# Kernel optimization log

Hardware: AMD Instinct MI355X
Metric: run time of the kernel (lower is better)

The kernel has to match this reference:

```python
import jax, jax.numpy as jnp
import numpy as np


def setup_inputs() -> dict:
    key = jax.random.key(0)
    x = jax.random.normal(key, (4, 4096, 64), dtype=jnp.float32)
    return {"x": x}


def reference(x) -> jnp.ndarray:
    # self-attention with q = k = v = x, shape [B, S, D]
    d = x.shape[-1]
    scale = 1.0 / jnp.sqrt(jnp.asarray(d, dtype=x.dtype))
    logits = jnp.einsum('bqd,bkd->bqk', x, x) * scale  # [B, S, S]
    attn = jax.nn.softmax(logits, axis=-1)
    return jnp.einsum('bqk,bkd->bqd', attn, x)
```

## Files before the change

kernel.cpp:

```cpp
#include <hip/hip_runtime.h>
#include <cstdint>


#define SB 4096
#define DDIM 64

typedef __attribute__((ext_vector_type(16))) float f32x16;
typedef __attribute__((ext_vector_type(8)))  float f32x8;
typedef __attribute__((ext_vector_type(4)))  float f32x4;
typedef __attribute__((ext_vector_type(8)))  short bf16x8;

static __device__ __forceinline__ unsigned short bf16_rne(float f) {
  union { float f; uint32_t u; } v; v.f = f;
  uint32_t u = v.u + 0x7FFFu + ((v.u >> 16) & 1u);
  return (unsigned short)(u >> 16);
}
static __device__ __forceinline__ float bf16_tof(unsigned short h) {
  union { uint32_t u; float f; } v; v.u = ((uint32_t)h) << 16;
  return v.f;
}
static __device__ __forceinline__ f32x16 MFMA(bf16x8 a, bf16x8 b, f32x16 c) {
  return __builtin_amdgcn_mfma_f32_32x32x16_bf16(a, b, c, 0, 0, 0);
}

#define KSTRIDE 272
#define VSTRIDE 144
#define VOFF    8704
#define WREG    17920

__global__ __launch_bounds__(512, 1)
void sdpa_kernel(const float* __restrict__ x, float* __restrict__ out) {
  __shared__ __align__(16) char smem[143360];
  const int tid  = threadIdx.x;
  const int wv   = tid >> 6;
  const int lane = tid & 63;
  const int l31  = lane & 31;
  const int h5   = lane >> 5;
  const int bid  = blockIdx.x;
  const int b    = bid >> 6;
  const int q0   = (bid & 63) << 6;
  const float* __restrict__ xb = x + (size_t)b * (SB * DDIM);
  char* __restrict__ wl = smem + (size_t)wv * WREG;

  const float NEG = -3.0e38f;

  bf16x8 qh[2][4], ql[2][4];
#pragma unroll
  for (int qf = 0; qf < 2; ++qf) {
#pragma unroll
    for (int dc = 0; dc < 4; ++dc) {
      const float* p = xb + (size_t)(q0 + qf * 32 + l31) * DDIM + dc * 16 + h5 * 8;
      f32x4 a = *(const f32x4*)p;
      f32x4 c = *(const f32x4*)(p + 4);
      float v[8] = {a[0], a[1], a[2], a[3], c[0], c[1], c[2], c[3]};
#pragma unroll
      for (int j = 0; j < 8; ++j) {
        float sv = v[j] * 0.125f;
        unsigned short hi = bf16_rne(sv);
        qh[qf][dc][j] = (short)hi;
        ql[qf][dc][j] = (short)bf16_rne(sv - bf16_tof(hi));
      }
    }
  }

  f32x16 ot[2][2] = {};
  float mrun[2] = {NEG, NEG};
  float lrun[2] = {0.f, 0.f};

  const int kv0 = wv * (SB / 8);
  const int r0  = (lane >> 3) * 4;
  const int d0g = (lane & 7) * 8;

  const int vc  = r0 >> 4;
  const int vko = r0 & 15;
  const int vsA = ((vko >> 2) & 1) * 8 + ((vko >> 3) & 1) * 4;
  const uint32_t vcolb = (uint32_t)(vc * 16 + vsA) * 2;

#pragma unroll 1
  for (int st = 0; st < 16; ++st) {
    const int krow0 = kv0 + st * 32;

    bf16x8 hv[4], lv[4];
#pragma unroll
    for (int i = 0; i < 4; ++i) {
      f32x8 t = *(const f32x8*)(xb + (size_t)(krow0 + r0 + i) * DDIM + d0g);
#pragma unroll
      for (int j = 0; j < 8; ++j) {
        unsigned short hi = bf16_rne(t[j]);
        hv[i][j] = (short)hi;
        lv[i][j] = (short)bf16_rne(t[j] - bf16_tof(hi));
      }
      const int row = r0 + i;
      *(bf16x8*)(wl + row * KSTRIDE + d0g * 2)       = hv[i];
      *(bf16x8*)(wl + row * KSTRIDE + 128 + d0g * 2) = lv[i];
    }
#pragma unroll
    for (int dd = 0; dd < 8; ++dd) {
      const int d = d0g + dd;
      const uint32_t sw = ((uint32_t)((d >> 3) & 7)) << 4;
      char* rb = wl + VOFF + (uint32_t)d * VSTRIDE;
      short4 pa = make_short4(hv[0][dd], hv[1][dd], hv[2][dd], hv[3][dd]);
      short4 pb = make_short4(lv[0][dd], lv[1][dd], lv[2][dd], lv[3][dd]);
      *(short4*)(rb + (vcolb ^ sw))          = pa;
      *(short4*)(rb + ((64 + vcolb) ^ sw))   = pb;
    }

    bf16x8 kh[4], kl[4];
    {
      char* krow = wl + l31 * KSTRIDE;
#pragma unroll
      for (int dc = 0; dc < 4; ++dc) {
        const uint32_t off = (uint32_t)(dc * 32 + h5 * 16);
        kh[dc] = *(bf16x8*)(krow + off);
        kl[dc] = *(bf16x8*)(krow + 128 + off);
      }
    }
    f32x16 s0 = {}, s1 = {};
#pragma unroll
    for (int dc = 0; dc < 4; ++dc) {
      s0 = MFMA(kh[dc], qh[0][dc], s0);
      s1 = MFMA(kh[dc], qh[1][dc], s1);
      s0 = MFMA(kh[dc], ql[0][dc], s0);
      s1 = MFMA(kh[dc], ql[1][dc], s1);
      s0 = MFMA(kl[dc], qh[0][dc], s0);
      s1 = MFMA(kl[dc], qh[1][dc], s1);
    }

    bf16x8 ph[2][2], pl[2][2];
#pragma unroll
    for (int qf = 0; qf < 2; ++qf) {
      f32x16 sv = qf ? s1 : s0;
      float pm = sv[0];
#pragma unroll
      for (int r = 1; r < 16; ++r) pm = fmaxf(pm, sv[r]);
      pm = fmaxf(pm, __shfl_xor(pm, 32));
      const float mnew = fmaxf(mrun[qf], pm);
      const float corr = __expf(mrun[qf] - mnew);
      mrun[qf] = mnew;
      lrun[qf] *= corr;
#pragma unroll
      for (int df = 0; df < 2; ++df)
#pragma unroll
        for (int r = 0; r < 16; ++r) ot[qf][df][r] *= corr;
      float p[16]; float ps = 0.f;
#pragma unroll
      for (int r = 0; r < 16; ++r) { p[r] = __expf(sv[r] - mnew); ps += p[r]; }
      lrun[qf] += ps;
#pragma unroll
      for (int c = 0; c < 2; ++c)
#pragma unroll
        for (int j = 0; j < 8; ++j) {
          float pv = p[c * 8 + j];
          unsigned short hi = bf16_rne(pv);
          ph[qf][c][j] = (short)hi;
          pl[qf][c][j] = (short)bf16_rne(pv - bf16_tof(hi));
        }
    }

#pragma unroll
    for (int df = 0; df < 2; ++df) {
      const int d = df * 32 + l31;
      char* rb = wl + VOFF + (uint32_t)d * VSTRIDE;
      const uint32_t sw = ((uint32_t)((d >> 3) & 7)) << 4;
      bf16x8 vh[2], vl2[2];
#pragma unroll
      for (int c = 0; c < 2; ++c) {
        const uint32_t off = (uint32_t)(c * 32 + h5 * 16);
        vh[c]  = *(bf16x8*)(rb + (off ^ sw));
        vl2[c] = *(bf16x8*)(rb + ((64 + off) ^ sw));
      }
#pragma unroll
      for (int qf = 0; qf < 2; ++qf)
#pragma unroll
        for (int c = 0; c < 2; ++c) {
          ot[qf][df] = MFMA(vh[c],  ph[qf][c], ot[qf][df]);
          ot[qf][df] = MFMA(vh[c],  pl[qf][c], ot[qf][df]);
          ot[qf][df] = MFMA(vl2[c], ph[qf][c], ot[qf][df]);
        }
    }
  }

#pragma unroll
  for (int qf = 0; qf < 2; ++qf) lrun[qf] += __shfl_xor(lrun[qf], 32);

  __syncthreads();
  if (wv > 0) {
    char* rbase = smem + (size_t)(wv - 1) * 17408 + (size_t)lane * 272;
#pragma unroll
    for (int qf = 0; qf < 2; ++qf)
#pragma unroll
      for (int df = 0; df < 2; ++df)
#pragma unroll
        for (int t = 0; t < 4; ++t) {
          f32x4 o = { ot[qf][df][t*4+0], ot[qf][df][t*4+1],
                      ot[qf][df][t*4+2], ot[qf][df][t*4+3] };
          *(f32x4*)(rbase + (qf * 128 + df * 64 + t * 16)) = o;
        }
    f32x4 stv = { mrun[0], lrun[0], mrun[1], lrun[1] };
    *(f32x4*)(rbase + 256) = stv;
  }
  __syncthreads();
  if (wv == 0) {
#pragma unroll 1
    for (int w = 1; w < 8; ++w) {
      char* rbase = smem + (size_t)(w - 1) * 17408 + (size_t)lane * 272;
      f32x4 stv = *(f32x4*)(rbase + 256);
#pragma unroll
      for (int qf = 0; qf < 2; ++qf) {
        const float mw = stv[qf * 2 + 0];
        const float lw = stv[qf * 2 + 1];
        const float mn = fmaxf(mrun[qf], mw);
        const float f0 = __expf(mrun[qf] - mn);
        const float f1 = __expf(mw - mn);
        mrun[qf] = mn;
        lrun[qf] = lrun[qf] * f0 + lw * f1;
#pragma unroll
        for (int df = 0; df < 2; ++df)
#pragma unroll
          for (int t = 0; t < 4; ++t) {
            f32x4 o = *(f32x4*)(rbase + (qf * 128 + df * 64 + t * 16));
#pragma unroll
            for (int e = 0; e < 4; ++e)
              ot[qf][df][t*4+e] = ot[qf][df][t*4+e] * f0 + o[e] * f1;
          }
      }
    }
#pragma unroll
    for (int qf = 0; qf < 2; ++qf) {
      const float inv = 1.0f / lrun[qf];
      const size_t rowoff = ((size_t)b * SB + q0 + qf * 32 + l31) * DDIM;
#pragma unroll
      for (int df = 0; df < 2; ++df)
#pragma unroll
        for (int t = 0; t < 4; ++t) {
          const int dbase = df * 32 + t * 8 + h5 * 4;
          f32x4 o = { ot[qf][df][t*4+0] * inv, ot[qf][df][t*4+1] * inv,
                      ot[qf][df][t*4+2] * inv, ot[qf][df][t*4+3] * inv };
          *(f32x4*)(out + rowoff + dbase) = o;
        }
    }
  }
}

extern "C" void kernel_launch(void* const* d_in, const int* in_sizes, int n_in,
                              void* d_out, int out_size, void* d_ws, size_t ws_size,
                              hipStream_t stream) {
  (void)in_sizes; (void)n_in; (void)out_size; (void)d_ws; (void)ws_size;
  const float* x = (const float*)d_in[0];
  float* o = (float*)d_out;
  sdpa_kernel<<<dim3(256), dim3(512), 0, stream>>>(x, o);
}
```

Before: 125.9 us.

## Precompute bf16 hi/lo split K and transposed V into workspace

Adds a precompute kernel that converts x once into split bf16 hi/lo K rows and transposed V arrays in a workspace buffer. The main attention kernel then loads MFMA operands straight from global memory, with no per-tile conversion, LDS staging or transposes, and remaps blocks so that each XCD works on a single batch for L2 locality. The work per block drops, but it costs an extra launch, 8MB of workspace traffic and global loads with no LDS reuse. If the workspace is too small, the old kernel runs instead.

```diff
diff --git a/kernel.cpp b/kernel.cpp
--- a/kernel.cpp
+++ b/kernel.cpp
@@ -23,13 +23,257 @@
   return __builtin_amdgcn_mfma_f32_32x32x16_bf16(a, b, c, 0, 0, 0);
 }
 
+#define KF_BYTES  (4u << 20)
+#define VT_BYTES  (2u << 20)
+#define WS_NEEDED (8u << 20)
+
+__device__ __constant__ int g_koff[16] = {0,1,2,3, 8,9,10,11, 4,5,6,7, 12,13,14,15};
+
+__global__ __launch_bounds__(256)
+void precompute_kernel(const float* __restrict__ x, char* __restrict__ ws) {
+  const int bid = blockIdx.x;
+  const int tid = threadIdx.x;
+  char* __restrict__ kfmt = ws;
+  char* __restrict__ vthi = ws + KF_BYTES;
+  char* __restrict__ vtlo = ws + KF_BYTES + VT_BYTES;
+  if (bid < 512) {
+    const int t   = bid * 256 + tid;
+    const int row = t >> 3;
+    const int seg = t & 7;
+    f32x8 v = *(const f32x8*)(x + (size_t)row * 64 + seg * 8);
+    bf16x8 h, l;
+#pragma unroll
+    for (int j = 0; j < 8; ++j) {
+      unsigned short hi = bf16_rne(v[j]);
+      h[j] = (short)hi;
+      l[j] = (short)bf16_rne(v[j] - bf16_tof(hi));
+    }
+    char* dst = kfmt + (size_t)row * 256 + seg * 16;
+    *(bf16x8*)dst         = h;
+    *(bf16x8*)(dst + 128) = l;
+  } else {
+    const int w = (bid - 512) * 4 + (tid >> 6);
+    const int b = w >> 8;
+    const int c = w & 255;
+    const int d = tid & 63;
+    unsigned short hs[16], ls[16];
+#pragma unroll
+    for (int s = 0; s < 16; ++s) {
+      const int k = c * 16 + g_koff[s];
+      float v = x[((size_t)(b * SB + k)) * 64 + d];
+      hs[s] = bf16_rne(v);
+      ls[s] = bf16_rne(v - bf16_tof(hs[s]));
+    }
+    bf16x8 h0, h1, l0, l1;
+#pragma unroll
+    for (int j = 0; j < 8; ++j) {
+      h0[j] = (short)hs[j];     h1[j] = (short)hs[j + 8];
+      l0[j] = (short)ls[j];     l1[j] = (short)ls[j + 8];
+    }
+    char* dh = vthi + (size_t)(b * 64 + d) * 8192 + c * 32;
+    char* dl = vtlo + (size_t)(b * 64 + d) * 8192 + c * 32;
+    *(bf16x8*)dh = h0; *(bf16x8*)(dh + 16) = h1;
+    *(bf16x8*)dl = l0; *(bf16x8*)(dl + 16) = l1;
+  }
+}
+
+__global__ __launch_bounds__(512, 2)
+void sdpa_main(const float* __restrict__ x, const char* __restrict__ ws,
+               float* __restrict__ out) {
+  __shared__ __align__(16) char smem[121856];
+  const int tid  = threadIdx.x;
+  const int wv   = tid >> 6;
+  const int lane = tid & 63;
+  const int l31  = lane & 31;
+  const int h5   = lane >> 5;
+
+  const int p    = blockIdx.x;
+  const int xcd  = p & 7;
+  const int slot = p >> 3;
+  const int b    = xcd >> 1;
+  const int q0   = ((xcd & 1) * 32 + slot) * 64;
+
+  const float* __restrict__ xb = x + (size_t)b * (SB * DDIM);
+  const char* __restrict__ kfmt = ws;
+  const char* __restrict__ vthi = ws + KF_BYTES;
+  const char* __restrict__ vtlo = ws + KF_BYTES + VT_BYTES;
+
+  const float NEG = -3.0e38f;
+
+  bf16x8 qh[2][4], ql[2][4];
+#pragma unroll
+  for (int qf = 0; qf < 2; ++qf) {
+#pragma unroll
+    for (int dc = 0; dc < 4; ++dc) {
+      const float* ptr = xb + (size_t)(q0 + qf * 32 + l31) * DDIM + dc * 16 + h5 * 8;
+      f32x4 a = *(const f32x4*)ptr;
+      f32x4 c = *(const f32x4*)(ptr + 4);
+      float v[8] = {a[0], a[1], a[2], a[3], c[0], c[1], c[2], c[3]};
+#pragma unroll
+      for (int j = 0; j < 8; ++j) {
+        float sv = v[j] * 0.125f;
+        unsigned short hi = bf16_rne(sv);
+        qh[qf][dc][j] = (short)hi;
+        ql[qf][dc][j] = (short)bf16_rne(sv - bf16_tof(hi));
+      }
+    }
+  }
+
+  f32x16 ot[2][2] = {};
+  float mrun[2] = {NEG, NEG};
+  float lrun[2] = {0.f, 0.f};
+
+  const int kv0 = wv * (SB / 8);
+
+  const char* kbase = kfmt + (size_t)(b * SB + kv0 + l31) * 256 + h5 * 16;
+  const char* vbh   = vthi + (size_t)(b * 64 + l31) * 8192 + (size_t)kv0 * 2 + h5 * 16;
+  const char* vbl   = vtlo + (size_t)(b * 64 + l31) * 8192 + (size_t)kv0 * 2 + h5 * 16;
+
+#pragma unroll 1
+  for (int st = 0; st < 16; ++st) {
+    bf16x8 kh[4], kl[4];
+#pragma unroll
+    for (int dc = 0; dc < 4; ++dc) {
+      kh[dc] = *(const bf16x8*)(kbase + dc * 32);
+      kl[dc] = *(const bf16x8*)(kbase + 128 + dc * 32);
+    }
+
+    f32x16 s0 = {}, s1 = {};
+#pragma unroll
+    for (int dc = 0; dc < 4; ++dc) {
+      s0 = MFMA(kh[dc], qh[0][dc], s0);
+      s1 = MFMA(kh[dc], qh[1][dc], s1);
+      s0 = MFMA(kh[dc], ql[0][dc], s0);
+      s1 = MFMA(kh[dc], ql[1][dc], s1);
+      s0 = MFMA(kl[dc], qh[0][dc], s0);
+      s1 = MFMA(kl[dc], qh[1][dc], s1);
+    }
+
+    bf16x8 vh[2][2], vl[2][2];
+#pragma unroll
+    for (int df = 0; df < 2; ++df)
+#pragma unroll
+      for (int c = 0; c < 2; ++c) {
+        vh[df][c] = *(const bf16x8*)(vbh + (size_t)df * (32 * 8192) + c * 32);
+        vl[df][c] = *(const bf16x8*)(vbl + (size_t)df * (32 * 8192) + c * 32);
+      }
+
+    bf16x8 ph[2][2], pl[2][2];
+#pragma unroll
+    for (int qf = 0; qf < 2; ++qf) {
+      f32x16 sv = qf ? s1 : s0;
+      float pm = sv[0];
+#pragma unroll
+      for (int r = 1; r < 16; ++r) pm = fmaxf(pm, sv[r]);
+      pm = fmaxf(pm, __shfl_xor(pm, 32));
+      const float mnew = fmaxf(mrun[qf], pm);
+      const float corr = __expf(mrun[qf] - mnew);
+      mrun[qf] = mnew;
+      lrun[qf] *= corr;
+#pragma unroll
+      for (int df = 0; df < 2; ++df)
+#pragma unroll
+        for (int r = 0; r < 16; ++r) ot[qf][df][r] *= corr;
+      float pv[16]; float ps = 0.f;
+#pragma unroll
+      for (int r = 0; r < 16; ++r) { pv[r] = __expf(sv[r] - mnew); ps += pv[r]; }
+      lrun[qf] += ps;
+#pragma unroll
+      for (int c = 0; c < 2; ++c)
+#pragma unroll
+        for (int j = 0; j < 8; ++j) {
+          float pvv = pv[c * 8 + j];
+          unsigned short hi = bf16_rne(pvv);
+          ph[qf][c][j] = (short)hi;
+          pl[qf][c][j] = (short)bf16_rne(pvv - bf16_tof(hi));
+        }
+    }
+
+#pragma unroll
+    for (int df = 0; df < 2; ++df)
+#pragma unroll
+      for (int qf = 0; qf < 2; ++qf)
+#pragma unroll
+        for (int c = 0; c < 2; ++c) {
+          ot[qf][df] = MFMA(vh[df][c], ph[qf][c], ot[qf][df]);
+          ot[qf][df] = MFMA(vh[df][c], pl[qf][c], ot[qf][df]);
+          ot[qf][df] = MFMA(vl[df][c], ph[qf][c], ot[qf][df]);
+        }
+
+    kbase += 32 * 256;
+    vbh   += 64;
+    vbl   += 64;
+  }
+
+#pragma unroll
+  for (int qf = 0; qf < 2; ++qf) lrun[qf] += __shfl_xor(lrun[qf], 32);
+
+  __syncthreads();
+  if (wv > 0) {
+    char* rbase = smem + (size_t)(wv - 1) * 17408 + (size_t)lane * 272;
+#pragma unroll
+    for (int qf = 0; qf < 2; ++qf)
+#pragma unroll
+      for (int df = 0; df < 2; ++df)
+#pragma unroll
+        for (int t = 0; t < 4; ++t) {
+          f32x4 o = { ot[qf][df][t*4+0], ot[qf][df][t*4+1],
+                      ot[qf][df][t*4+2], ot[qf][df][t*4+3] };
+          *(f32x4*)(rbase + (qf * 128 + df * 64 + t * 16)) = o;
+        }
+    f32x4 stv = { mrun[0], lrun[0], mrun[1], lrun[1] };
+    *(f32x4*)(rbase + 256) = stv;
+  }
+  __syncthreads();
+  if (wv == 0) {
+#pragma unroll 1
+    for (int w = 1; w < 8; ++w) {
+      char* rbase = smem + (size_t)(w - 1) * 17408 + (size_t)lane * 272;
+      f32x4 stv = *(f32x4*)(rbase + 256);
+#pragma unroll
+      for (int qf = 0; qf < 2; ++qf) {
+        const float mw = stv[qf * 2 + 0];
+        const float lw = stv[qf * 2 + 1];
+        const float mn = fmaxf(mrun[qf], mw);
+        const float f0 = __expf(mrun[qf] - mn);
+        const float f1 = __expf(mw - mn);
+        mrun[qf] = mn;
+        lrun[qf] = lrun[qf] * f0 + lw * f1;
+#pragma unroll
+        for (int df = 0; df < 2; ++df)
+#pragma unroll
+          for (int t = 0; t < 4; ++t) {
+            f32x4 o = *(f32x4*)(rbase + (qf * 128 + df * 64 + t * 16));
+#pragma unroll
+            for (int e = 0; e < 4; ++e)
+              ot[qf][df][t*4+e] = ot[qf][df][t*4+e] * f0 + o[e] * f1;
+          }
+      }
+    }
+#pragma unroll
+    for (int qf = 0; qf < 2; ++qf) {
+      const float inv = 1.0f / lrun[qf];
+      const size_t rowoff = ((size_t)b * SB + q0 + qf * 32 + l31) * DDIM;
+#pragma unroll
+      for (int df = 0; df < 2; ++df)
+#pragma unroll
+        for (int t = 0; t < 4; ++t) {
+          const int dbase = df * 32 + t * 8 + h5 * 4;
+          f32x4 o = { ot[qf][df][t*4+0] * inv, ot[qf][df][t*4+1] * inv,
+                      ot[qf][df][t*4+2] * inv, ot[qf][df][t*4+3] * inv };
+          *(f32x4*)(out + rowoff + dbase) = o;
+        }
+    }
+  }
+}
+
 #define KSTRIDE 272
 #define VSTRIDE 144
 #define VOFF    8704
 #define WREG    17920
 
 __global__ __launch_bounds__(512, 1)
-void sdpa_kernel(const float* __restrict__ x, float* __restrict__ out) {
+void sdpa_fb(const float* __restrict__ x, float* __restrict__ out) {
   __shared__ __align__(16) char smem[143360];
   const int tid  = threadIdx.x;
   const int wv   = tid >> 6;
@@ -41,17 +285,16 @@
   const int q0   = (bid & 63) << 6;
   const float* __restrict__ xb = x + (size_t)b * (SB * DDIM);
   char* __restrict__ wl = smem + (size_t)wv * WREG;
-
   const float NEG = -3.0e38f;
 
   bf16x8 qh[2][4], ql[2][4];
 #pragma unroll
-  for (int qf = 0; qf < 2; ++qf) {
+  for (int qf = 0; qf < 2; ++qf)
 #pragma unroll
     for (int dc = 0; dc < 4; ++dc) {
-      const float* p = xb + (size_t)(q0 + qf * 32 + l31) * DDIM + dc * 16 + h5 * 8;
-      f32x4 a = *(const f32x4*)p;
-      f32x4 c = *(const f32x4*)(p + 4);
+      const float* ptr = xb + (size_t)(q0 + qf * 32 + l31) * DDIM + dc * 16 + h5 * 8;
+      f32x4 a = *(const f32x4*)ptr;
+      f32x4 c = *(const f32x4*)(ptr + 4);
       float v[8] = {a[0], a[1], a[2], a[3], c[0], c[1], c[2], c[3]};
 #pragma unroll
       for (int j = 0; j < 8; ++j) {
@@ -61,16 +304,13 @@
         ql[qf][dc][j] = (short)bf16_rne(sv - bf16_tof(hi));
       }
     }
-  }
 
   f32x16 ot[2][2] = {};
   float mrun[2] = {NEG, NEG};
   float lrun[2] = {0.f, 0.f};
-
   const int kv0 = wv * (SB / 8);
   const int r0  = (lane >> 3) * 4;
   const int d0g = (lane & 7) * 8;
-
   const int vc  = r0 >> 4;
   const int vko = r0 & 15;
   const int vsA = ((vko >> 2) & 1) * 8 + ((vko >> 3) & 1) * 4;
@@ -79,7 +319,6 @@
 #pragma unroll 1
   for (int st = 0; st < 16; ++st) {
     const int krow0 = kv0 + st * 32;
-
     bf16x8 hv[4], lv[4];
 #pragma unroll
     for (int i = 0; i < 4; ++i) {
@@ -101,8 +340,8 @@
       char* rb = wl + VOFF + (uint32_t)d * VSTRIDE;
       short4 pa = make_short4(hv[0][dd], hv[1][dd], hv[2][dd], hv[3][dd]);
       short4 pb = make_short4(lv[0][dd], lv[1][dd], lv[2][dd], lv[3][dd]);
-      *(short4*)(rb + (vcolb ^ sw))          = pa;
-      *(short4*)(rb + ((64 + vcolb) ^ sw))   = pb;
+      *(short4*)(rb + (vcolb ^ sw))        = pa;
+      *(short4*)(rb + ((64 + vcolb) ^ sw)) = pb;
     }
 
     bf16x8 kh[4], kl[4];
@@ -142,18 +381,18 @@
       for (int df = 0; df < 2; ++df)
 #pragma unroll
         for (int r = 0; r < 16; ++r) ot[qf][df][r] *= corr;
-      float p[16]; float ps = 0.f;
-#pragma unroll
-      for (int r = 0; r < 16; ++r) { p[r] = __expf(sv[r] - mnew); ps += p[r]; }
+      float pv[16]; float ps = 0.f;
+#pragma unroll
+      for (int r = 0; r < 16; ++r) { pv[r] = __expf(sv[r] - mnew); ps += pv[r]; }
       lrun[qf] += ps;
 #pragma unroll
       for (int c = 0; c < 2; ++c)
 #pragma unroll
         for (int j = 0; j < 8; ++j) {
-          float pv = p[c * 8 + j];
-          unsigned short hi = bf16_rne(pv);
+          float pvv = pv[c * 8 + j];
+          unsigned short hi = bf16_rne(pvv);
           ph[qf][c][j] = (short)hi;
-          pl[qf][c][j] = (short)bf16_rne(pv - bf16_tof(hi));
+          pl[qf][c][j] = (short)bf16_rne(pvv - bf16_tof(hi));
         }
     }
 
@@ -245,8 +484,13 @@
 extern "C" void kernel_launch(void* const* d_in, const int* in_sizes, int n_in,
                               void* d_out, int out_size, void* d_ws, size_t ws_size,
                               hipStream_t stream) {
-  (void)in_sizes; (void)n_in; (void)out_size; (void)d_ws; (void)ws_size;
+  (void)in_sizes; (void)n_in; (void)out_size;
   const float* x = (const float*)d_in[0];
   float* o = (float*)d_out;
-  sdpa_kernel<<<dim3(256), dim3(512), 0, stream>>>(x, o);
-}
+  if (ws_size >= (size_t)WS_NEEDED) {
+    precompute_kernel<<<dim3(768), dim3(256), 0, stream>>>(x, (char*)d_ws);
+    sdpa_main<<<dim3(256), dim3(512), 0, stream>>>(x, (const char*)d_ws, o);
+  } else {
+    sdpa_fb<<<dim3(256), dim3(512), 0, stream>>>(x, o);
+  }
+}
```

Result: slower. 129.1 us (+2.5%).
